# Performance work log

Hardware: AMD Instinct MI355X
Metric: run time of the kernel (lower is better)

Reference implementation:

```python
import jax, jax.numpy as jnp
import numpy as np

B, N, M, C1, C2 = 16, 4096, 1024, 128, 256
MLP0, MLP1 = 256, 256
IN_CH = C1 + C2
EPS = 1e-5


def setup_inputs() -> dict:
    key = jax.random.key(0)
    ks = jax.random.split(key, 6)
    return {
        "xyz1": jax.random.normal(ks[0], (B, 3, N), jnp.float32),
        "xyz2": jax.random.normal(ks[1], (B, 3, M), jnp.float32),
        "points1": jax.random.normal(ks[2], (B, C1, N), jnp.float32),
        "points2": jax.random.normal(ks[3], (B, C2, M), jnp.float32),
        "W1": jax.random.normal(ks[4], (MLP0, IN_CH), jnp.float32) * (1.0 / np.sqrt(IN_CH)),
        "gamma1": jnp.ones((MLP0,), jnp.float32),
        "beta1": jnp.zeros((MLP0,), jnp.float32),
        "W2": jax.random.normal(ks[5], (MLP1, MLP0), jnp.float32) * (1.0 / np.sqrt(MLP0)),
        "gamma2": jnp.ones((MLP1,), jnp.float32),
        "beta2": jnp.zeros((MLP1,), jnp.float32),
    }


def _batchnorm(x, gamma, beta):
    # x: (B, N, C); normalize per channel over batch*length (training-mode BN, biased var)
    mean = jnp.mean(x, axis=(0, 1))
    var = jnp.mean((x - mean) ** 2, axis=(0, 1))
    return (x - mean) * jax.lax.rsqrt(var + EPS) * gamma + beta


def reference(xyz1, xyz2, points1, points2, W1, gamma1, beta1, W2, gamma2, beta2):
    p1 = jnp.swapaxes(xyz1, 1, 2)  # (B, N, 3)
    p2 = jnp.swapaxes(xyz2, 1, 2)  # (B, M, 3)
    # squared pairwise distances (B, N, M); squaring preserves 3-NN ordering,
    # and the original squares the euclidean dist before weighting anyway
    d2 = jnp.sum((p1[:, :, None, :] - p2[:, None, :, :]) ** 2, axis=-1)
    neg_d2, idx = jax.lax.top_k(-d2, 3)  # 3 smallest distances
    dist2 = jnp.maximum(-neg_d2, 1e-10)  # (B, N, 3)
    inv = 1.0 / dist2
    weight = inv / jnp.sum(inv, axis=-1, keepdims=True)  # (B, N, 3)
    f2 = jnp.swapaxes(points2, 1, 2)  # (B, M, C2)
    b, n, k = idx.shape
    gathered = jnp.take_along_axis(
        f2, idx.reshape(b, n * k)[:, :, None], axis=1
    ).reshape(b, n, k, -1)  # (B, N, 3, C2)
    interp = jnp.einsum("bnk,bnkc->bnc", weight, gathered)  # (B, N, C2)
    feat = jnp.concatenate([interp, jnp.swapaxes(points1, 1, 2)], axis=-1)  # (B, N, C1+C2)
    h = jnp.einsum("bnc,oc->bno", feat, W1)  # conv1d k=1, no bias
    h = jax.nn.relu(_batchnorm(h, gamma1, beta1))
    h = jnp.einsum("bnc,oc->bno", h, W2)
    h = jax.nn.relu(_batchnorm(h, gamma2, beta2))
    return jnp.swapaxes(h, 1, 2)  # (B, MLP1, N), channel-first like torch
```

## Files before the change

### kernel.cpp

```cpp
#include <hip/hip_runtime.h>

typedef unsigned short u16;
typedef unsigned int u32;

#define BB 16
#define NN 4096
#define MM 1024
#define C1V 128
#define C2V 256
#define EPSV 1e-5f
#define INV_CNT (1.0f/65536.0f)
#define NREP 32

typedef __attribute__((ext_vector_type(8))) short bf16x8;
typedef __attribute__((ext_vector_type(4))) float f32x4;

static __device__ __forceinline__ u16 f2b(float f) {
  u32 u = __float_as_uint(f);
  u32 r = (u + 0x7FFFu + ((u >> 16) & 1u)) >> 16;
  return (u16)r;
}
static __device__ __forceinline__ float b2f(u16 s) {
  return __uint_as_float(((u32)s) << 16);
}

#define GLD_LDS16(gp, lp)                                                      \
  __builtin_amdgcn_global_load_lds(                                            \
      (const __attribute__((address_space(1))) void*)(gp),                     \
      (__attribute__((address_space(3))) void*)(lp), 16, 0, 0)

__device__ __forceinline__ void tcast_tile(const float* __restrict__ in,
                                           u16* __restrict__ out, int C, int P,
                                           int p0, int c0, int b,
                                           float (*tile)[33]) {
  int tx = threadIdx.x & 31, ty = threadIdx.x >> 5;
  const float* ib = in + (size_t)b * C * P;
  u16* ob = out + (size_t)b * P * C;
#pragma unroll
  for (int i = 0; i < 4; ++i)
    tile[ty + i * 8][tx] = ib[(size_t)(c0 + ty + i * 8) * P + p0 + tx];
  __syncthreads();
#pragma unroll
  for (int i = 0; i < 4; ++i)
    ob[(size_t)(p0 + ty + i * 8) * C + c0 + tx] = f2b(tile[tx][ty + i * 8]);
}

__global__ __launch_bounds__(256) void prep_kernel(
    const float* __restrict__ xyz1, const float* __restrict__ xyz2,
    float* __restrict__ pd, int* __restrict__ pi,
    const float* __restrict__ points1, const float* __restrict__ points2,
    u16* __restrict__ p1t, u16* __restrict__ p2t,
    const float* __restrict__ W1, const float* __restrict__ W2,
    u16* __restrict__ W1b, u16* __restrict__ W2b,
    float* __restrict__ statsZero) {
  __shared__ float4 cand[256];
  __shared__ float tile[32][33];
  int bx = blockIdx.x;
  int t = threadIdx.x;

  if (bx < 512) {
    int c = bx & 3;
    int qt = (bx >> 2) & 7;
    int b = bx >> 5;
    const float* x2b = xyz2 + b * 3 * MM;
    {
      float x = x2b[c * 256 + t];
      float y = x2b[MM + c * 256 + t];
      float z = x2b[2 * MM + c * 256 + t];
      cand[t] = make_float4(x, y, z, x * x + y * y + z * z);
    }
    __syncthreads();
    const float* x1b = xyz1 + b * 3 * NN;
    int n0 = qt * 512 + t;
    int n1 = n0 + 256;
    float px0 = x1b[n0], py0 = x1b[NN + n0], pz0 = x1b[2 * NN + n0];
    float px1 = x1b[n1], py1 = x1b[NN + n1], pz1 = x1b[2 * NN + n1];
    const float INF = 3.4e38f;
    float k00 = INF, k01 = INF, k02 = INF;
    float k10 = INF, k11 = INF, k12 = INF;
    int j00 = 0, j01 = 0, j02 = 0;
    int j10 = 0, j11 = 0, j12 = 0;
#pragma unroll 8
    for (int m = 0; m < 256; ++m) {
      float4 cd = cand[m];
      {
        float dot = fmaf(px0, cd.x, fmaf(py0, cd.y, pz0 * cd.z));
        float key = fmaf(-2.0f, dot, cd.w);
        bool c0 = key < k00, c1 = key < k01, c2 = key < k02;
        k02 = c1 ? k01 : (c2 ? key : k02);
        j02 = c1 ? j01 : (c2 ? m : j02);
        k01 = c0 ? k00 : (c1 ? key : k01);
        j01 = c0 ? j00 : (c1 ? m : j01);
        k00 = c0 ? key : k00;
        j00 = c0 ? m : j00;
      }
      {
        float dot = fmaf(px1, cd.x, fmaf(py1, cd.y, pz1 * cd.z));
        float key = fmaf(-2.0f, dot, cd.w);
        bool c0 = key < k10, c1 = key < k11, c2 = key < k12;
        k12 = c1 ? k11 : (c2 ? key : k12);
        j12 = c1 ? j11 : (c2 ? m : j12);
        k11 = c0 ? k10 : (c1 ? key : k11);
        j11 = c0 ? j10 : (c1 ? m : j11);
        k10 = c0 ? key : k10;
        j10 = c0 ? m : j10;
      }
    }
    float pn0 = px0 * px0 + py0 * py0 + pz0 * pz0;
    float pn1 = px1 * px1 + py1 * py1 + pz1 * pz1;
    int gq0 = b * NN + n0;
    int gq1 = b * NN + n1;
    int base = c << 8;
    ((float4*)pd)[(size_t)c * 65536 + gq0] =
        make_float4(fmaxf(k00 + pn0, 1e-10f), fmaxf(k01 + pn0, 1e-10f),
                    fmaxf(k02 + pn0, 1e-10f), 0.0f);
    ((int4*)pi)[(size_t)c * 65536 + gq0] =
        make_int4(base + j00, base + j01, base + j02, 0);
    ((float4*)pd)[(size_t)c * 65536 + gq1] =
        make_float4(fmaxf(k10 + pn1, 1e-10f), fmaxf(k11 + pn1, 1e-10f),
                    fmaxf(k12 + pn1, 1e-10f), 0.0f);
    ((int4*)pi)[(size_t)c * 65536 + gq1] =
        make_int4(base + j10, base + j11, base + j12, 0);
  } else if (bx < 1152) {
    int i = (bx - 512) * 256 + t;
    if (i < 98304) W1b[i] = f2b(W1[i]);
    else if (i < 163840) W2b[i - 98304] = f2b(W2[i - 98304]);
  } else if (bx < 1184) {
    ((float4*)statsZero)[(bx - 1152) * 256 + t] =
        make_float4(0.f, 0.f, 0.f, 0.f);
  } else if (bx < 5280) {
    int local = bx - 1184;
    int pt = local & 31, ct = (local >> 5) & 7, b = local >> 8;
    tcast_tile(points2, p2t, C2V, MM, pt * 32, ct * 32, b, tile);
  } else {
    int local = bx - 5280;
    int pt = local & 127, ct = (local >> 7) & 3, b = local >> 9;
    tcast_tile(points1, p1t, C1V, NN, pt * 32, ct * 32, b, tile);
  }
}

template <int K, int NTILES, bool INTERP, bool STATS, bool OUTB, bool BNA>
__global__ __launch_bounds__(256) void gemm_mfma(
    const u16* __restrict__ A, int lda, const u16* __restrict__ B, int ldb,
    void* __restrict__ out, const u16* __restrict__ G,
    const float* __restrict__ pd, const int* __restrict__ pi,
    float* __restrict__ statsOut, const float* __restrict__ statsInR,
    const float* __restrict__ gamma, const float* __restrict__ beta) {
  __shared__ u16 smem[16384];
  __shared__ float wsh[128][3];
  __shared__ int ish[128][3];
  __shared__ float scA[256], shA[256];

  int t = threadIdx.x;
  int w = t >> 6, l = t & 63;
  int n0;
  if (NTILES > 0) {
    int p = blockIdx.x;
    int batch = ((p & 7) << 1) | ((p >> 3) & 1);
    int nt = p >> 4;
    n0 = (batch * NTILES + nt) * 128;
  } else {
    n0 = blockIdx.x * 128;
  }
  int o0 = blockIdx.y * 128;

  if (INTERP) {
    if (t < 128) {
      int gq = n0 + t;
      float4 d0 = ((const float4*)pd)[gq];
      int4 ii0 = ((const int4*)pi)[gq];
      float a0 = d0.x, a1 = d0.y, a2 = d0.z;
      int b0 = ii0.x, b1 = ii0.y, b2 = ii0.z;
#pragma unroll
      for (int c = 1; c < 4; ++c) {
        float4 dc = ((const float4*)pd)[(size_t)c * 65536 + gq];
        int4 ic = ((const int4*)pi)[(size_t)c * 65536 + gq];
        float kv[3] = {dc.x, dc.y, dc.z};
        int jv[3] = {ic.x, ic.y, ic.z};
#pragma unroll
        for (int j = 0; j < 3; ++j) {
          float key = kv[j];
          int idx = jv[j];
          bool c0 = key < a0, c1 = key < a1, c2 = key < a2;
          a2 = c1 ? a1 : (c2 ? key : a2);
          b2 = c1 ? b1 : (c2 ? idx : b2);
          a1 = c0 ? a0 : (c1 ? key : a1);
          b1 = c0 ? b0 : (c1 ? idx : b1);
          a0 = c0 ? key : a0;
          b0 = c0 ? idx : b0;
        }
      }
      float v0 = 1.0f / a0, v1 = 1.0f / a1, v2 = 1.0f / a2;
      float s = 1.0f / (v0 + v1 + v2);
      wsh[t][0] = v0 * s; wsh[t][1] = v1 * s; wsh[t][2] = v2 * s;
      ish[t][0] = b0;     ish[t][1] = b1;     ish[t][2] = b2;
    }
  }
  if (BNA) {
    float s = 0.0f, qq = 0.0f;
#pragma unroll
    for (int r = 0; r < NREP; ++r) {
      s += statsInR[r * 512 + t];
      qq += statsInR[r * 512 + 256 + t];
    }
    float mean = s * INV_CNT;
    float var = qq * INV_CNT - mean * mean;
    float sc = rsqrtf(var + EPSV) * gamma[t];
    scA[t] = sc;
    shA[t] = beta[t] - mean * sc;
  }

  int wm = w & 1, wn = w >> 1;
  int lr = l >> 2, lc = l & 3;
  int q = l >> 4, m = l & 15;

  f32x4 acc[4][4] = {};
  u16* As = smem;
  u16* Bs = smem + 4096;

  const u16* arow = A + (size_t)n0 * lda;
  const u16* brow = B + (size_t)o0 * ldb;

#pragma unroll
  for (int kt = 0; kt < K; kt += 32) {
    __syncthreads();
#pragma unroll
    for (int r = 0; r < 2; ++r) {
      int row = r * 64 + w * 16 + lr;
      if (BNA) {
        union { uint4 u; u16 s[8]; } v, o;
        v.u = *(const uint4*)(arow + (size_t)row * lda + kt + lc * 8);
        int cb = kt + lc * 8;
#pragma unroll
        for (int j = 0; j < 8; ++j) {
          float f = fmaf(b2f(v.s[j]), scA[cb + j], shA[cb + j]);
          o.s[j] = f2b(fmaxf(f, 0.0f));
        }
        *(uint4*)(As + row * 32 + lc * 8) = o.u;
      } else {
        GLD_LDS16(arow + (size_t)row * lda + kt + lc * 8, As + row * 32 + lc * 8);
      }
    }
#pragma unroll
    for (int r = 0; r < 2; ++r) {
      int row = r * 64 + w * 16 + lr;
      GLD_LDS16(brow + (size_t)row * ldb + kt + lc * 8, Bs + row * 32 + lc * 8);
    }
    __syncthreads();
    bf16x8 af[4], bf[4];
#pragma unroll
    for (int i = 0; i < 4; ++i)
      af[i] = *(const bf16x8*)(As + (wm * 64 + i * 16 + m) * 32 + q * 8);
#pragma unroll
    for (int j = 0; j < 4; ++j)
      bf[j] = *(const bf16x8*)(Bs + (wn * 64 + j * 16 + m) * 32 + q * 8);
#pragma unroll
    for (int i = 0; i < 4; ++i)
#pragma unroll
      for (int j = 0; j < 4; ++j)
        acc[i][j] =
            __builtin_amdgcn_mfma_f32_16x16x32_bf16(af[i], bf[j], acc[i][j], 0, 0, 0);
  }

  if (INTERP) {
    __syncthreads();
    int b = n0 >> 12;
    int rl = t >> 1, half = t & 1, rx = rl & 7;
    float w0 = wsh[rl][0], w1 = wsh[rl][1], w2 = wsh[rl][2];
    const u16* g0 = G + ((size_t)(b * 1024 + ish[rl][0])) * 256 + o0 + half * 64;
    const u16* g1 = G + ((size_t)(b * 1024 + ish[rl][1])) * 256 + o0 + half * 64;
    const u16* g2 = G + ((size_t)(b * 1024 + ish[rl][2])) * 256 + o0 + half * 64;
#pragma unroll
    for (int c8 = 0; c8 < 8; ++c8) {
      bf16x8 v0 = *(const bf16x8*)(g0 + c8 * 8);
      bf16x8 v1 = *(const bf16x8*)(g1 + c8 * 8);
      bf16x8 v2 = *(const bf16x8*)(g2 + c8 * 8);
      union { uint4 u; u16 s[8]; } o;
#pragma unroll
      for (int e = 0; e < 8; ++e) {
        float f = w0 * b2f((u16)v0[e]) + w1 * b2f((u16)v1[e]) +
                  w2 * b2f((u16)v2[e]);
        o.s[e] = f2b(f);
      }
      int ch = (half * 8 + c8) ^ rx;
      *(uint4*)(smem + rl * 128 + ch * 8) = o.u;
    }
    __syncthreads();
#pragma unroll
    for (int i = 0; i < 4; ++i)
#pragma unroll
      for (int reg = 0; reg < 4; ++reg) {
        int row = wm * 64 + i * 16 + q * 4 + reg;
        int rxr = row & 7;
#pragma unroll
        for (int j = 0; j < 4; ++j) {
          int col = wn * 64 + j * 16 + m;
          int off = row * 128 + (((col >> 3) ^ rxr) << 3) + (col & 7);
          acc[i][j][reg] += b2f(smem[off]);
        }
      }
  }

  if (STATS) {
    int rep = blockIdx.x & (NREP - 1);
#pragma unroll
    for (int j = 0; j < 4; ++j) {
      float s = 0.0f, ss = 0.0f;
#pragma unroll
      for (int i = 0; i < 4; ++i)
#pragma unroll
        for (int reg = 0; reg < 4; ++reg) {
          float v = acc[i][j][reg];
          s += v;
          ss += v * v;
        }
      s += __shfl_down(s, 32); ss += __shfl_down(ss, 32);
      s += __shfl_down(s, 16); ss += __shfl_down(ss, 16);
      if (l < 16) {
        int c = o0 + wn * 64 + j * 16 + l;
        atomicAdd(&statsOut[rep * 512 + c], s);
        atomicAdd(&statsOut[rep * 512 + 256 + c], ss);
      }
    }
  }

  if (OUTB) {
    __syncthreads();
#pragma unroll
    for (int i = 0; i < 4; ++i)
#pragma unroll
      for (int reg = 0; reg < 4; ++reg) {
        int row = wm * 64 + i * 16 + q * 4 + reg;
#pragma unroll
        for (int j = 0; j < 4; ++j)
          smem[row * 128 + wn * 64 + j * 16 + m] = f2b(acc[i][j][reg]);
      }
    __syncthreads();
    u16* outp = (u16*)out;
    int rbase = w * 32 + (l >> 4);
    int seg = l & 15;
#pragma unroll
    for (int itr = 0; itr < 8; ++itr) {
      int row = rbase + itr * 4;
      uint4 v = *(const uint4*)(smem + row * 128 + seg * 8);
      *(uint4*)(outp + (size_t)(n0 + row) * 256 + o0 + seg * 8) = v;
    }
  } else {
#pragma unroll
    for (int i = 0; i < 4; ++i) {
      int gr = n0 + wm * 64 + i * 16 + q * 4;
#pragma unroll
      for (int reg = 0; reg < 4; ++reg)
#pragma unroll
        for (int j = 0; j < 4; ++j) {
          int gc = o0 + wn * 64 + j * 16 + m;
          ((float*)out)[(size_t)(gr + reg) * 256 + gc] = acc[i][j][reg];
        }
    }
  }
}

__global__ __launch_bounds__(256) void gemm2_64(
    const u16* __restrict__ A, const u16* __restrict__ B,
    u16* __restrict__ out, float* __restrict__ statsOut,
    const float* __restrict__ statsInR, const float* __restrict__ gamma,
    const float* __restrict__ beta) {
  __shared__ __align__(16) u16 smem[16384];
  __shared__ float scA[256], shA[256];
  int t = threadIdx.x;
  int w = t >> 6, l = t & 63;
  int n0 = blockIdx.x * 64;

  {
    float s = 0.0f, qq = 0.0f;
#pragma unroll
    for (int r = 0; r < NREP; ++r) {
      s += statsInR[r * 512 + t];
      qq += statsInR[r * 512 + 256 + t];
    }
    float mean = s * INV_CNT;
    float var = qq * INV_CNT - mean * mean;
    float sc = rsqrtf(var + EPSV) * gamma[t];
    scA[t] = sc;
    shA[t] = beta[t] - mean * sc;
  }

  int q = l >> 4, m = l & 15;
  int sr = l >> 2, lc = l & 3;

  f32x4 acc[4][4] = {};
  u16* As = smem;
  u16* Bs = smem + 2048;
  const u16* arow = A + (size_t)n0 * 256;

#pragma unroll
  for (int kt = 0; kt < 256; kt += 32) {
    __syncthreads();
    {
      int row = w * 16 + sr;
      union { uint4 u; u16 s[8]; } v, o;
      v.u = *(const uint4*)(arow + (size_t)row * 256 + kt + lc * 8);
      int cb = kt + lc * 8;
#pragma unroll
      for (int j = 0; j < 8; ++j) {
        float f = fmaf(b2f(v.s[j]), scA[cb + j], shA[cb + j]);
        o.s[j] = f2b(fmaxf(f, 0.0f));
      }
      *(uint4*)(As + row * 32 + lc * 8) = o.u;
    }
#pragma unroll
    for (int r = 0; r < 4; ++r) {
      int row = r * 64 + w * 16 + sr;
      GLD_LDS16(B + (size_t)row * 256 + kt + lc * 8, Bs + row * 32 + lc * 8);
    }
    __syncthreads();
    bf16x8 af[4], bf[4];
#pragma unroll
    for (int i = 0; i < 4; ++i)
      af[i] = *(const bf16x8*)(As + (i * 16 + m) * 32 + q * 8);
#pragma unroll
    for (int j = 0; j < 4; ++j)
      bf[j] = *(const bf16x8*)(Bs + (w * 64 + j * 16 + m) * 32 + q * 8);
#pragma unroll
    for (int i = 0; i < 4; ++i)
#pragma unroll
      for (int j = 0; j < 4; ++j)
        acc[i][j] =
            __builtin_amdgcn_mfma_f32_16x16x32_bf16(af[i], bf[j], acc[i][j], 0, 0, 0);
  }

  {
    int rep = blockIdx.x & (NREP - 1);
#pragma unroll
    for (int j = 0; j < 4; ++j) {
      float s = 0.0f, ss = 0.0f;
#pragma unroll
      for (int i = 0; i < 4; ++i)
#pragma unroll
        for (int reg = 0; reg < 4; ++reg) {
          float v = acc[i][j][reg];
          s += v;
          ss += v * v;
        }
      s += __shfl_down(s, 32); ss += __shfl_down(ss, 32);
      s += __shfl_down(s, 16); ss += __shfl_down(ss, 16);
      if (l < 16) {
        int c = w * 64 + j * 16 + l;
        atomicAdd(&statsOut[rep * 512 + c], s);
        atomicAdd(&statsOut[rep * 512 + 256 + c], ss);
      }
    }
  }

  __syncthreads();
#pragma unroll
  for (int i = 0; i < 4; ++i)
#pragma unroll
    for (int reg = 0; reg < 4; ++reg) {
      int row = i * 16 + q * 4 + reg;
#pragma unroll
      for (int j = 0; j < 4; ++j)
        smem[row * 256 + w * 64 + j * 16 + m] = f2b(acc[i][j][reg]);
    }
  __syncthreads();
  int rbase = t >> 5, seg = t & 31;
#pragma unroll
  for (int itr = 0; itr < 8; ++itr) {
    int row = rbase + itr * 8;
    uint4 v = *(const uint4*)(smem + row * 256 + seg * 8);
    *(uint4*)(out + (size_t)(n0 + row) * 256 + seg * 8) = v;
  }
}

__global__ __launch_bounds__(256) void bn2t_kernel(
    const u16* __restrict__ h2, const float* __restrict__ statsR,
    const float* __restrict__ gamma, const float* __restrict__ beta,
    float* __restrict__ out) {
  __shared__ float tile[32][33];
  __shared__ float sS[32], sH[32];
  int t = threadIdx.x;
  int tx = t & 31, ty = t >> 5;
  int n0 = blockIdx.x * 32, c0 = blockIdx.y * 32, b = blockIdx.z;
  if (t < 32) {
    int c = c0 + t;
    float s = 0.0f, qq = 0.0f;
#pragma unroll
    for (int r = 0; r < NREP; ++r) {
      s += statsR[r * 512 + c];
      qq += statsR[r * 512 + 256 + c];
    }
    float mean = s * INV_CNT;
    float var = qq * INV_CNT - mean * mean;
    float sc = rsqrtf(var + EPSV) * gamma[c];
    sS[t] = sc;
    sH[t] = beta[c] - mean * sc;
  }
  __syncthreads();
#pragma unroll
  for (int i = 0; i < 4; ++i) {
    int n = n0 + ty + i * 8;
    float v = b2f(h2[((size_t)b * NN + n) * 256 + c0 + tx]) * sS[tx] + sH[tx];
    tile[ty + i * 8][tx] = fmaxf(v, 0.0f);
  }
  __syncthreads();
#pragma unroll
  for (int i = 0; i < 4; ++i)
    out[((size_t)b * 256 + c0 + ty + i * 8) * NN + n0 + tx] = tile[tx][ty + i * 8];
}

extern "C" void kernel_launch(void* const* d_in, const int* in_sizes, int n_in,
                              void* d_out, int out_size, void* d_ws,
                              size_t ws_size, hipStream_t stream) {
  const float* xyz1    = (const float*)d_in[0];
  const float* xyz2    = (const float*)d_in[1];
  const float* points1 = (const float*)d_in[2];
  const float* points2 = (const float*)d_in[3];
  const float* W1      = (const float*)d_in[4];
  const float* gamma1  = (const float*)d_in[5];
  const float* beta1   = (const float*)d_in[6];
  const float* W2      = (const float*)d_in[7];
  const float* gamma2  = (const float*)d_in[8];
  const float* beta2   = (const float*)d_in[9];

  char* ws = (char*)d_ws;
  float* stats1R = (float*)(ws + 0);
  float* stats2R = (float*)(ws + 65536);
  u16*   W1b     = (u16*)(ws + 131072);
  u16*   W2b     = (u16*)(ws + 327680);
  u16*   p2t     = (u16*)(ws + 458752);
  u16*   p1t     = (u16*)(ws + 8847360);
  u16*   G       = (u16*)(ws + 25624576);
  u16*   h2b     = (u16*)(ws + 34013184);
  float* pd      = (float*)(ws + 67567616);
  int*   pi      = (int*)(ws + 71761920);
  u16*   h1b     = (u16*)d_out;
  float* out     = (float*)d_out;

  prep_kernel<<<13472, 256, 0, stream>>>(xyz1, xyz2, pd, pi, points1, points2,
                                         p1t, p2t, W1, W2, W1b, W2b, stats1R);
  gemm_mfma<256, 8, false, false, true, false><<<dim3(128, 2), 256, 0, stream>>>(
      p2t, 256, W1b, 384, G, nullptr, nullptr, nullptr, nullptr, nullptr,
      nullptr, nullptr);
  gemm_mfma<128, 32, true, true, true, false><<<dim3(512, 2), 256, 0, stream>>>(
      p1t, 128, W1b + 256, 384, h1b, G, pd, pi, stats1R, nullptr, nullptr,
      nullptr);
  gemm2_64<<<1024, 256, 0, stream>>>(h1b, W2b, h2b, stats2R, stats1R, gamma1,
                                     beta1);
  bn2t_kernel<<<dim3(128, 8, 16), 256, 0, stream>>>(h2b, stats2R, gamma2,
                                                    beta2, out);
}
```

Measured before the change: 227.8 us.

## Retile first MLP GEMM to full-width 64-row blocks and vectorize BN2 transpose

The fused interpolation+GEMM1 kernel moves from 128x128 tiles split across two column blocks to a dedicated 64-row by 256-column kernel. The 3-NN merge and the feature gather are now done once per point instead of once per column half, and each block writes full output rows. The final BN+ReLU transpose kernel switches to 64x64 tiles with 8-byte vector loads and float4 stores to cut per-element memory transactions. In exchange, each GEMM1 block reloads the whole W1 slice per k-step, and occupancy may change with the larger tiles.

```diff
diff --git a/kernel.cpp b/kernel.cpp
--- a/kernel.cpp
+++ b/kernel.cpp
@@ -139,18 +139,11 @@
   }
 }
 
-template <int K, int NTILES, bool INTERP, bool STATS, bool OUTB, bool BNA>
+template <int K, int NTILES, bool OUTB>
 __global__ __launch_bounds__(256) void gemm_mfma(
     const u16* __restrict__ A, int lda, const u16* __restrict__ B, int ldb,
-    void* __restrict__ out, const u16* __restrict__ G,
-    const float* __restrict__ pd, const int* __restrict__ pi,
-    float* __restrict__ statsOut, const float* __restrict__ statsInR,
-    const float* __restrict__ gamma, const float* __restrict__ beta) {
+    void* __restrict__ out) {
   __shared__ u16 smem[16384];
-  __shared__ float wsh[128][3];
-  __shared__ int ish[128][3];
-  __shared__ float scA[256], shA[256];
-
   int t = threadIdx.x;
   int w = t >> 6, l = t & 63;
   int n0;
@@ -164,52 +157,6 @@
   }
   int o0 = blockIdx.y * 128;
 
-  if (INTERP) {
-    if (t < 128) {
-      int gq = n0 + t;
-      float4 d0 = ((const float4*)pd)[gq];
-      int4 ii0 = ((const int4*)pi)[gq];
-      float a0 = d0.x, a1 = d0.y, a2 = d0.z;
-      int b0 = ii0.x, b1 = ii0.y, b2 = ii0.z;
-#pragma unroll
-      for (int c = 1; c < 4; ++c) {
-        float4 dc = ((const float4*)pd)[(size_t)c * 65536 + gq];
-        int4 ic = ((const int4*)pi)[(size_t)c * 65536 + gq];
-        float kv[3] = {dc.x, dc.y, dc.z};
-        int jv[3] = {ic.x, ic.y, ic.z};
-#pragma unroll
-        for (int j = 0; j < 3; ++j) {
-          float key = kv[j];
-          int idx = jv[j];
-          bool c0 = key < a0, c1 = key < a1, c2 = key < a2;
-          a2 = c1 ? a1 : (c2 ? key : a2);
-          b2 = c1 ? b1 : (c2 ? idx : b2);
-          a1 = c0 ? a0 : (c1 ? key : a1);
-          b1 = c0 ? b0 : (c1 ? idx : b1);
-          a0 = c0 ? key : a0;
-          b0 = c0 ? idx : b0;
-        }
-      }
-      float v0 = 1.0f / a0, v1 = 1.0f / a1, v2 = 1.0f / a2;
-      float s = 1.0f / (v0 + v1 + v2);
-      wsh[t][0] = v0 * s; wsh[t][1] = v1 * s; wsh[t][2] = v2 * s;
-      ish[t][0] = b0;     ish[t][1] = b1;     ish[t][2] = b2;
-    }
-  }
-  if (BNA) {
-    float s = 0.0f, qq = 0.0f;
-#pragma unroll
-    for (int r = 0; r < NREP; ++r) {
-      s += statsInR[r * 512 + t];
-      qq += statsInR[r * 512 + 256 + t];
-    }
-    float mean = s * INV_CNT;
-    float var = qq * INV_CNT - mean * mean;
-    float sc = rsqrtf(var + EPSV) * gamma[t];
-    scA[t] = sc;
-    shA[t] = beta[t] - mean * sc;
-  }
-
   int wm = w & 1, wn = w >> 1;
   int lr = l >> 2, lc = l & 3;
   int q = l >> 4, m = l & 15;
@@ -227,19 +174,7 @@
 #pragma unroll
     for (int r = 0; r < 2; ++r) {
       int row = r * 64 + w * 16 + lr;
-      if (BNA) {
-        union { uint4 u; u16 s[8]; } v, o;
-        v.u = *(const uint4*)(arow + (size_t)row * lda + kt + lc * 8);
-        int cb = kt + lc * 8;
-#pragma unroll
-        for (int j = 0; j < 8; ++j) {
-          float f = fmaf(b2f(v.s[j]), scA[cb + j], shA[cb + j]);
-          o.s[j] = f2b(fmaxf(f, 0.0f));
-        }
-        *(uint4*)(As + row * 32 + lc * 8) = o.u;
-      } else {
-        GLD_LDS16(arow + (size_t)row * lda + kt + lc * 8, As + row * 32 + lc * 8);
-      }
+      GLD_LDS16(arow + (size_t)row * lda + kt + lc * 8, As + row * 32 + lc * 8);
     }
 #pragma unroll
     for (int r = 0; r < 2; ++r) {
@@ -262,14 +197,133 @@
             __builtin_amdgcn_mfma_f32_16x16x32_bf16(af[i], bf[j], acc[i][j], 0, 0, 0);
   }
 
-  if (INTERP) {
-    __syncthreads();
+  if (OUTB) {
+    __syncthreads();
+#pragma unroll
+    for (int i = 0; i < 4; ++i)
+#pragma unroll
+      for (int reg = 0; reg < 4; ++reg) {
+        int row = wm * 64 + i * 16 + q * 4 + reg;
+#pragma unroll
+        for (int j = 0; j < 4; ++j)
+          smem[row * 128 + wn * 64 + j * 16 + m] = f2b(acc[i][j][reg]);
+      }
+    __syncthreads();
+    u16* outp = (u16*)out;
+    int rbase = w * 32 + (l >> 4);
+    int seg = l & 15;
+#pragma unroll
+    for (int itr = 0; itr < 8; ++itr) {
+      int row = rbase + itr * 4;
+      uint4 v = *(const uint4*)(smem + row * 128 + seg * 8);
+      *(uint4*)(outp + (size_t)(n0 + row) * 256 + o0 + seg * 8) = v;
+    }
+  } else {
+#pragma unroll
+    for (int i = 0; i < 4; ++i) {
+      int gr = n0 + wm * 64 + i * 16 + q * 4;
+#pragma unroll
+      for (int reg = 0; reg < 4; ++reg)
+#pragma unroll
+        for (int j = 0; j < 4; ++j) {
+          int gc = o0 + wn * 64 + j * 16 + m;
+          ((float*)out)[(size_t)(gr + reg) * 256 + gc] = acc[i][j][reg];
+        }
+    }
+  }
+}
+
+__global__ __launch_bounds__(256) void gemm1_64(
+    const u16* __restrict__ A, const u16* __restrict__ B,
+    u16* __restrict__ out, const u16* __restrict__ G,
+    const float* __restrict__ pd, const int* __restrict__ pi,
+    float* __restrict__ statsOut) {
+  __shared__ __align__(16) u16 smem[16384];
+  __shared__ float wsh[64][3];
+  __shared__ int ish[64][3];
+  int t = threadIdx.x;
+  int w = t >> 6, l = t & 63;
+  int p = blockIdx.x;
+  int batch = ((p & 7) << 1) | ((p >> 3) & 1);
+  int nt = p >> 4;
+  int n0 = batch * NN + nt * 64;
+
+  if (t < 64) {
+    int gq = n0 + t;
+    float4 d0 = ((const float4*)pd)[gq];
+    int4 ii0 = ((const int4*)pi)[gq];
+    float a0 = d0.x, a1 = d0.y, a2 = d0.z;
+    int b0 = ii0.x, b1 = ii0.y, b2 = ii0.z;
+#pragma unroll
+    for (int c = 1; c < 4; ++c) {
+      float4 dc = ((const float4*)pd)[(size_t)c * 65536 + gq];
+      int4 ic = ((const int4*)pi)[(size_t)c * 65536 + gq];
+      float kv[3] = {dc.x, dc.y, dc.z};
+      int jv[3] = {ic.x, ic.y, ic.z};
+#pragma unroll
+      for (int j = 0; j < 3; ++j) {
+        float key = kv[j];
+        int idx = jv[j];
+        bool c0 = key < a0, c1 = key < a1, c2 = key < a2;
+        a2 = c1 ? a1 : (c2 ? key : a2);
+        b2 = c1 ? b1 : (c2 ? idx : b2);
+        a1 = c0 ? a0 : (c1 ? key : a1);
+        b1 = c0 ? b0 : (c1 ? idx : b1);
+        a0 = c0 ? key : a0;
+        b0 = c0 ? idx : b0;
+      }
+    }
+    float v0 = 1.0f / a0, v1 = 1.0f / a1, v2 = 1.0f / a2;
+    float s = 1.0f / (v0 + v1 + v2);
+    wsh[t][0] = v0 * s; wsh[t][1] = v1 * s; wsh[t][2] = v2 * s;
+    ish[t][0] = b0;     ish[t][1] = b1;     ish[t][2] = b2;
+  }
+
+  int q = l >> 4, m = l & 15;
+  int sr = l >> 2, lc = l & 3;
+
+  f32x4 acc[4][4] = {};
+  u16* As = smem;
+  u16* Bs = smem + 2048;
+  const u16* arow = A + (size_t)n0 * 128;
+
+#pragma unroll
+  for (int kt = 0; kt < 128; kt += 32) {
+    __syncthreads();
+    {
+      int row = w * 16 + sr;
+      GLD_LDS16(arow + (size_t)row * 128 + kt + lc * 8, As + row * 32 + lc * 8);
+    }
+#pragma unroll
+    for (int r = 0; r < 4; ++r) {
+      int row = r * 64 + w * 16 + sr;
+      GLD_LDS16(B + (size_t)row * 384 + kt + lc * 8, Bs + row * 32 + lc * 8);
+    }
+    __syncthreads();
+    bf16x8 af[4], bf[4];
+#pragma unroll
+    for (int i = 0; i < 4; ++i)
+      af[i] = *(const bf16x8*)(As + (i * 16 + m) * 32 + q * 8);
+#pragma unroll
+    for (int j = 0; j < 4; ++j)
+      bf[j] = *(const bf16x8*)(Bs + (w * 64 + j * 16 + m) * 32 + q * 8);
+#pragma unroll
+    for (int i = 0; i < 4; ++i)
+#pragma unroll
+      for (int j = 0; j < 4; ++j)
+        acc[i][j] =
+            __builtin_amdgcn_mfma_f32_16x16x32_bf16(af[i], bf[j], acc[i][j], 0, 0, 0);
+  }
+
+  __syncthreads();
+  {
     int b = n0 >> 12;
-    int rl = t >> 1, half = t & 1, rx = rl & 7;
+    int rl = t >> 2, qt = t & 3;
     float w0 = wsh[rl][0], w1 = wsh[rl][1], w2 = wsh[rl][2];
-    const u16* g0 = G + ((size_t)(b * 1024 + ish[rl][0])) * 256 + o0 + half * 64;
-    const u16* g1 = G + ((size_t)(b * 1024 + ish[rl][1])) * 256 + o0 + half * 64;
-    const u16* g2 = G + ((size_t)(b * 1024 + ish[rl][2])) * 256 + o0 + half * 64;
+    const u16* g0 = G + ((size_t)(b * 1024 + ish[rl][0])) * 256 + qt * 64;
+    const u16* g1 = G + ((size_t)(b * 1024 + ish[rl][1])) * 256 + qt * 64;
+    const u16* g2 = G + ((size_t)(b * 1024 + ish[rl][2])) * 256 + qt * 64;
+    int r3 = (rl >> 2) & 7;
 #pragma unroll
     for (int c8 = 0; c8 < 8; ++c8) {
       bf16x8 v0 = *(const bf16x8*)(g0 + c8 * 8);
@@ -282,152 +336,24 @@
                   w2 * b2f((u16)v2[e]);
         o.s[e] = f2b(f);
       }
-      int ch = (half * 8 + c8) ^ rx;
-      *(uint4*)(smem + rl * 128 + ch * 8) = o.u;
-    }
-    __syncthreads();
-#pragma unroll
-    for (int i = 0; i < 4; ++i)
-#pragma unroll
-      for (int reg = 0; reg < 4; ++reg) {
-        int row = wm * 64 + i * 16 + q * 4 + reg;
-        int rxr = row & 7;
-#pragma unroll
-        for (int j = 0; j < 4; ++j) {
-          int col = wn * 64 + j * 16 + m;
-          int off = row * 128 + (((col >> 3) ^ rxr) << 3) + (col & 7);
-          acc[i][j][reg] += b2f(smem[off]);
-        }
-      }
-  }
-
-  if (STATS) {
-    int rep = blockIdx.x & (NREP - 1);
-#pragma unroll
-    for (int j = 0; j < 4; ++j) {
-      float s = 0.0f, ss = 0.0f;
-#pragma unroll
-      for (int i = 0; i < 4; ++i)
-#pragma unroll
-        for (int reg = 0; reg < 4; ++reg) {
-          float v = acc[i][j][reg];
-          s += v;
-          ss += v * v;
-        }
-      s += __shfl_down(s, 32); ss += __shfl_down(ss, 32);
-      s += __shfl_down(s, 16); ss += __shfl_down(ss, 16);
-      if (l < 16) {
-        int c = o0 + wn * 64 + j * 16 + l;
-        atomicAdd(&statsOut[rep * 512 + c], s);
-        atomicAdd(&statsOut[rep * 512 + 256 + c], ss);
-      }
-    }
-  }
-
-  if (OUTB) {
-    __syncthreads();
-#pragma unroll
-    for (int i = 0; i < 4; ++i)
-#pragma unroll
-      for (int reg = 0; reg < 4; ++reg) {
-        int row = wm * 64 + i * 16 + q * 4 + reg;
-#pragma unroll
-        for (int j = 0; j < 4; ++j)
-          smem[row * 128 + wn * 64 + j * 16 + m] = f2b(acc[i][j][reg]);
-      }
-    __syncthreads();
-    u16* outp = (u16*)out;
-    int rbase = w * 32 + (l >> 4);
-    int seg = l & 15;
-#pragma unroll
-    for (int itr = 0; itr < 8; ++itr) {
-      int row = rbase + itr * 4;
-      uint4 v = *(const uint4*)(smem + row * 128 + seg * 8);
-      *(uint4*)(outp + (size_t)(n0 + row) * 256 + o0 + seg * 8) = v;
-    }
-  } else {
-#pragma unroll
-    for (int i = 0; i < 4; ++i) {
-      int gr = n0 + wm * 64 + i * 16 + q * 4;
-#pragma unroll
-      for (int reg = 0; reg < 4; ++reg)
-#pragma unroll
-        for (int j = 0; j < 4; ++j) {
-          int gc = o0 + wn * 64 + j * 16 + m;
-          ((float*)out)[(size_t)(gr + reg) * 256 + gc] = acc[i][j][reg];
-        }
-    }
-  }
-}
-
-__global__ __launch_bounds__(256) void gemm2_64(
-    const u16* __restrict__ A, const u16* __restrict__ B,
-    u16* __restrict__ out, float* __restrict__ statsOut,
-    const float* __restrict__ statsInR, const float* __restrict__ gamma,
-    const float* __restrict__ beta) {
-  __shared__ __align__(16) u16 smem[16384];
-  __shared__ float scA[256], shA[256];
-  int t = threadIdx.x;
-  int w = t >> 6, l = t & 63;
-  int n0 = blockIdx.x * 64;
-
-  {
-    float s = 0.0f, qq = 0.0f;
-#pragma unroll
-    for (int r = 0; r < NREP; ++r) {
-      s += statsInR[r * 512 + t];
-      qq += statsInR[r * 512 + 256 + t];
-    }
-    float mean = s * INV_CNT;
-    float var = qq * INV_CNT - mean * mean;
-    float sc = rsqrtf(var + EPSV) * gamma[t];
-    scA[t] = sc;
-    shA[t] = beta[t] - mean * sc;
-  }
-
-  int q = l >> 4, m = l & 15;
-  int sr = l >> 2, lc = l & 3;
-
-  f32x4 acc[4][4] = {};
-  u16* As = smem;
-  u16* Bs = smem + 2048;
-  const u16* arow = A + (size_t)n0 * 256;
-
-#pragma unroll
-  for (int kt = 0; kt < 256; kt += 32) {
-    __syncthreads();
-    {
-      int row = w * 16 + sr;
-      union { uint4 u; u16 s[8]; } v, o;
-      v.u = *(const uint4*)(arow + (size_t)row * 256 + kt + lc * 8);
-      int cb = kt + lc * 8;
-#pragma unroll
-      for (int j = 0; j < 8; ++j) {
-        float f = fmaf(b2f(v.s[j]), scA[cb + j], shA[cb + j]);
-        o.s[j] = f2b(fmaxf(f, 0.0f));
-      }
-      *(uint4*)(As + row * 32 + lc * 8) = o.u;
-    }
-#pragma unroll
-    for (int r = 0; r < 4; ++r) {
-      int row = r * 64 + w * 16 + sr;
-      GLD_LDS16(B + (size_t)row * 256 + kt + lc * 8, Bs + row * 32 + lc * 8);
-    }
-    __syncthreads();
-    bf16x8 af[4], bf[4];
-#pragma unroll
-    for (int i = 0; i < 4; ++i)
-      af[i] = *(const bf16x8*)(As + (i * 16 + m) * 32 + q * 8);
-#pragma unroll
-    for (int j = 0; j < 4; ++j)
-      bf[j] = *(const bf16x8*)(Bs + (w * 64 + j * 16 + m) * 32 + q * 8);
-#pragma unroll
-    for (int i = 0; i < 4; ++i)
-#pragma unroll
-      for (int j = 0; j < 4; ++j)
-        acc[i][j] =
-            __builtin_amdgcn_mfma_f32_16x16x32_bf16(af[i], bf[j], acc[i][j], 0, 0, 0);
-  }
+      int ch = (qt * 8 + c8) ^ r3;
+      *(uint4*)(smem + rl * 256 + ch * 8) = o.u;
+    }
+  }
+  __syncthreads();
+#pragma unroll
+  for (int i = 0; i < 4; ++i)
+#pragma unroll
+    for (int reg = 0; reg < 4; ++reg) {
+      int row = i * 16 + q * 4 + reg;
+      int rx = (row >> 2) & 7;
+#pragma unroll
+      for (int j = 0; j < 4; ++j) {
+        int col = w * 64 + j * 16 + m;
+        int off = row * 256 + (((col >> 3) ^ rx) << 3) + (col & 7);
+        acc[i][j][reg] += b2f(smem[off]);
+      }
+    }
 
   {
     int rep = blockIdx.x & (NREP - 1);
@@ -472,16 +398,127 @@
   }
 }
 
+__global__ __launch_bounds__(256) void gemm2_64(
+    const u16* __restrict__ A, const u16* __restrict__ B,
+    u16* __restrict__ out, float* __restrict__ statsOut,
+    const float* __restrict__ statsInR, const float* __restrict__ gamma,
+    const float* __restrict__ beta) {
+  __shared__ __align__(16) u16 smem[16384];
+  __shared__ float scA[256], shA[256];
+  int t = threadIdx.x;
+  int w = t >> 6, l = t & 63;
+  int n0 = blockIdx.x * 64;
+
+  {
+    float s = 0.0f, qq = 0.0f;
+#pragma unroll
+    for (int r = 0; r < NREP; ++r) {
+      s += statsInR[r * 512 + t];
+      qq += statsInR[r * 512 + 256 + t];
+    }
+    float mean = s * INV_CNT;
+    float var = qq * INV_CNT - mean * mean;
+    float sc = rsqrtf(var + EPSV) * gamma[t];
+    scA[t] = sc;
+    shA[t] = beta[t] - mean * sc;
+  }
+
+  int q = l >> 4, m = l & 15;
+  int sr = l >> 2, lc = l & 3;
+
+  f32x4 acc[4][4] = {};
+  u16* As = smem;
+  u16* Bs = smem + 2048;
+  const u16* arow = A + (size_t)n0 * 256;
+
+#pragma unroll
+  for (int kt = 0; kt < 256; kt += 32) {
+    __syncthreads();
+    {
+      int row = w * 16 + sr;
+      union { uint4 u; u16 s[8]; } v, o;
+      v.u = *(const uint4*)(arow + (size_t)row * 256 + kt + lc * 8);
+      int cb = kt + lc * 8;
+#pragma unroll
+      for (int j = 0; j < 8; ++j) {
+        float f = fmaf(b2f(v.s[j]), scA[cb + j], shA[cb + j]);
+        o.s[j] = f2b(fmaxf(f, 0.0f));
+      }
+      *(uint4*)(As + row * 32 + lc * 8) = o.u;
+    }
+#pragma unroll
+    for (int r = 0; r < 4; ++r) {
+      int row = r * 64 + w * 16 + sr;
+      GLD_LDS16(B + (size_t)row * 256 + kt + lc * 8, Bs + row * 32 + lc * 8);
+    }
+    __syncthreads();
+    bf16x8 af[4], bf[4];
+#pragma unroll
+    for (int i = 0; i < 4; ++i)
+      af[i] = *(const bf16x8*)(As + (i * 16 + m) * 32 + q * 8);
+#pragma unroll
+    for (int j = 0; j < 4; ++j)
+      bf[j] = *(const bf16x8*)(Bs + (w * 64 + j * 16 + m) * 32 + q * 8);
+#pragma unroll
+    for (int i = 0; i < 4; ++i)
+#pragma unroll
+      for (int j = 0; j < 4; ++j)
+        acc[i][j] =
+            __builtin_amdgcn_mfma_f32_16x16x32_bf16(af[i], bf[j], acc[i][j], 0, 0, 0);
+  }
+
+  {
+    int rep = blockIdx.x & (NREP - 1);
+#pragma unroll
+    for (int j = 0; j < 4; ++j) {
+      float s = 0.0f, ss = 0.0f;
+#pragma unroll
+      for (int i = 0; i < 4; ++i)
+#pragma unroll
+        for (int reg = 0; reg < 4; ++reg) {
+          float v = acc[i][j][reg];
+          s += v;
+          ss += v * v;
+        }
+      s += __shfl_down(s, 32); ss += __shfl_down(ss, 32);
+      s += __shfl_down(s, 16); ss += __shfl_down(ss, 16);
+      if (l < 16) {
+        int c = w * 64 + j * 16 + l;
+        atomicAdd(&statsOut[rep * 512 + c], s);
+        atomicAdd(&statsOut[rep * 512 + 256 + c], ss);
+      }
+    }
+  }
+
+  __syncthreads();
+#pragma unroll
+  for (int i = 0; i < 4; ++i)
+#pragma unroll
+    for (int reg = 0; reg < 4; ++reg) {
+      int row = i * 16 + q * 4 + reg;
+#pragma unroll
+      for (int j = 0; j < 4; ++j)
+        smem[row * 256 + w * 64 + j * 16 + m] = f2b(acc[i][j][reg]);
+    }
+  __syncthreads();
+  int rbase = t >> 5, seg = t & 31;
+#pragma unroll
+  for (int itr = 0; itr < 8; ++itr) {
+    int row = rbase + itr * 8;
+    uint4 v = *(const uint4*)(smem + row * 256 + seg * 8);
+    *(uint4*)(out + (size_t)(n0 + row) * 256 + seg * 8) = v;
+  }
+}
+
 __global__ __launch_bounds__(256) void bn2t_kernel(
     const u16* __restrict__ h2, const float* __restrict__ statsR,
     const float* __restrict__ gamma, const float* __restrict__ beta,
     float* __restrict__ out) {
-  __shared__ float tile[32][33];
-  __shared__ float sS[32], sH[32];
+  __shared__ float tile[64][65];
+  __shared__ float sS[64], sH[64];
   int t = threadIdx.x;
-  int tx = t & 31, ty = t >> 5;
-  int n0 = blockIdx.x * 32, c0 = blockIdx.y * 32, b = blockIdx.z;
-  if (t < 32) {
+  int n0 = blockIdx.x * 64, c0 = blockIdx.y * 64, b = blockIdx.z;
+  if (t < 64) {
     int c = c0 + t;
     float s = 0.0f, qq = 0.0f;
 #pragma unroll
@@ -496,16 +533,26 @@
     sH[t] = beta[c] - mean * sc;
   }
   __syncthreads();
+  int tx = t & 15, ty = t >> 4;
 #pragma unroll
   for (int i = 0; i < 4; ++i) {
-    int n = n0 + ty + i * 8;
-    float v = b2f(h2[((size_t)b * NN + n) * 256 + c0 + tx]) * sS[tx] + sH[tx];
-    tile[ty + i * 8][tx] = fmaxf(v, 0.0f);
-  }
-  __syncthreads();
-#pragma unroll
-  for (int i = 0; i < 4; ++i)
-    out[((size_t)b * 256 + c0 + ty + i * 8) * NN + n0 + tx] = tile[tx][ty + i * 8];
+    int n = ty + i * 16;
+    uint2 v = *(const uint2*)(h2 + ((size_t)b * NN + n0 + n) * 256 + c0 + tx * 4);
+    int c = tx * 4;
+    tile[n][c + 0] = fmaxf(fmaf(b2f((u16)(v.x & 0xffff)), sS[c + 0], sH[c + 0]), 0.0f);
+    tile[n][c + 1] = fmaxf(fmaf(b2f((u16)(v.x >> 16)),    sS[c + 1], sH[c + 1]), 0.0f);
+    tile[n][c + 2] = fmaxf(fmaf(b2f((u16)(v.y & 0xffff)), sS[c + 2], sH[c + 2]), 0.0f);
+    tile[n][c + 3] = fmaxf(fmaf(b2f((u16)(v.y >> 16)),    sS[c + 3], sH[c + 3]), 0.0f);
+  }
+  __syncthreads();
+#pragma unroll
+  for (int i = 0; i < 4; ++i) {
+    int c = ty + i * 16;
+    int nq = tx * 4;
+    float4 o4 = make_float4(tile[nq + 0][c], tile[nq + 1][c],
+                            tile[nq + 2][c], tile[nq + 3][c]);
+    *(float4*)(out + ((size_t)(b * 256 + c0 + c)) * NN + n0 + nq) = o4;
+  }
 }
 
 extern "C" void kernel_launch(void* const* d_in, const int* in_sizes, int n_in,
@@ -538,14 +585,11 @@
 
   prep_kernel<<<13472, 256, 0, stream>>>(xyz1, xyz2, pd, pi, points1, points2,
                                          p1t, p2t, W1, W2, W1b, W2b, stats1R);
-  gemm_mfma<256, 8, false, false, true, false><<<dim3(128, 2), 256, 0, stream>>>(
-      p2t, 256, W1b, 384, G, nullptr, nullptr, nullptr, nullptr, nullptr,
-      nullptr, nullptr);
-  gemm_mfma<128, 32, true, true, true, false><<<dim3(512, 2), 256, 0, stream>>>(
-      p1t, 128, W1b + 256, 384, h1b, G, pd, pi, stats1R, nullptr, nullptr,
-      nullptr);
+  gemm_mfma<256, 8, true><<<dim3(128, 2), 256, 0, stream>>>(p2t, 256, W1b, 384,
+                                                            G);
+  gemm1_64<<<1024, 256, 0, stream>>>(p1t, W1b + 256, h1b, G, pd, pi, stats1R);
   gemm2_64<<<1024, 256, 0, stream>>>(h1b, W2b, h2b, stats2R, stats1R, gamma1,
                                      beta1);
-  bn2t_kernel<<<dim3(128, 8, 16), 256, 0, stream>>>(h2b, stats2R, gamma2,
-                                                    beta2, out);
-}
+  bn2t_kernel<<<dim3(64, 4, 16), 256, 0, stream>>>(h2b, stats2R, gamma2,
+                                                   beta2, out);
+}
```

Measured after the change: 229.5 us. No clear change (+0.7%).
